# Optimization experiments

Measured on AMD Instinct MI355X. Metric: run time of the kernel, lower is better.

Reference implementation:

```python
import jax, jax.numpy as jnp
import numpy as np

B, N, Th, Td, Tw, Tp = 8, 3000, 24, 12, 24, 12
T2a, T2b, K = 64, 32, 3  # hidden temporal dims of the two STBlocks, Cheb order


def _laplacian(A):
    # PyG ChebConv with lambda_max=None -> lambda_max=2.0, sym normalization:
    # L_hat = 2L/lambda_max - I = -D^{-1/2} A D^{-1/2} with zero diagonal
    Aod = A * (1.0 - jnp.eye(A.shape[0], dtype=A.dtype))
    deg = Aod.sum(axis=1)
    dinv = jnp.where(deg > 0, deg ** -0.5, 0.0)
    return -(dinv[:, None] * Aod * dinv[None, :])


def _cheb(x, L, W, b):
    # Chebyshev graph conv, K=3. x: (B,N,Cin), L: (N,N), W: (K,Cin,Cout), b: (Cout,)
    Tx0 = x
    Tx1 = jnp.einsum('nm,bmi->bni', L, Tx0)
    Tx2 = 2.0 * jnp.einsum('nm,bmi->bni', L, Tx1) - Tx0
    out = (jnp.einsum('bni,io->bno', Tx0, W[0])
           + jnp.einsum('bni,io->bno', Tx1, W[1])
           + jnp.einsum('bni,io->bno', Tx2, W[2]))
    return out + b


def _tconv(x, w, b):
    # Conv1d(1, 1, 3, padding=1) over last axis. x: (B,N,T), w: (3,), b: scalar
    xp = jnp.pad(x, ((0, 0), (0, 0), (1, 1)))
    return w[0] * xp[..., :-2] + w[1] * xp[..., 1:-1] + w[2] * xp[..., 2:] + b


def _stblock(x, L, W, bg, cw, cb):
    x = jax.nn.relu(_cheb(x, L, W, bg))
    return jax.nn.relu(_tconv(x, cw, cb))


def _branch(X, L, W1, b1, c1w, c1b, W2, b2, c2w, c2b, WD, bD):
    x = X.reshape(X.shape[0], X.shape[1], X.shape[3])  # (B,N,T)
    x = _stblock(x, L, W1, b1, c1w, c1b)  # (B,N,64)
    x = _stblock(x, L, W2, b2, c2w, c2b)  # (B,N,32)
    return jax.nn.relu(x @ WD + bD)       # (B,N,Tp); forward only uses LinearD


def setup_inputs() -> dict:
    ks = jax.random.split(jax.random.key(0), 48)
    it = iter(range(48))

    def nrm(shape, s=1.0):
        return jax.random.normal(ks[next(it)], shape, jnp.float32) * s

    Xh = nrm((B, N, 1, Th))
    Xd = nrm((B, N, 1, Td))
    Xw = nrm((B, N, 1, Tw))
    u = jax.random.uniform(ks[next(it)], (N, N))
    w = jax.random.uniform(ks[next(it)], (N, N))
    A = jnp.where(u < 0.01, w, 0.0)
    A = 0.5 * (A + A.T)

    def gcn_p(ti, to):
        return nrm((K, ti, to), (2.0 / (ti + to)) ** 0.5), jnp.zeros((to,), jnp.float32)

    def conv_p():
        return nrm((K,), 0.4), nrm((), 0.1)

    Wh1, bh1 = gcn_p(Th, T2a); ch1w, ch1b = conv_p()
    Wh2, bh2 = gcn_p(T2a, T2b); ch2w, ch2b = conv_p()
    Wd1, bd1 = gcn_p(Td, T2a); cd1w, cd1b = conv_p()
    Wd2, bd2 = gcn_p(T2a, T2b); cd2w, cd2b = conv_p()
    Ww1, bw1 = gcn_p(Tw, T2a); cw1w, cw1b = conv_p()
    Ww2, bw2 = gcn_p(T2a, T2b); cw2w, cw2b = conv_p()
    WD = nrm((T2b, Tp), (2.0 / (T2b + Tp)) ** 0.5)
    bD = jnp.zeros((Tp,), jnp.float32)
    Fh = jax.random.uniform(ks[next(it)], (Tp,), jnp.float32)
    Fd = jax.random.uniform(ks[next(it)], (Tp,), jnp.float32)
    Fw = jax.random.uniform(ks[next(it)], (Tp,), jnp.float32)

    return dict(Xh=Xh, Xd=Xd, Xw=Xw, A=A,
                Wh1=Wh1, bh1=bh1, ch1w=ch1w, ch1b=ch1b, Wh2=Wh2, bh2=bh2, ch2w=ch2w, ch2b=ch2b,
                Wd1=Wd1, bd1=bd1, cd1w=cd1w, cd1b=cd1b, Wd2=Wd2, bd2=bd2, cd2w=cd2w, cd2b=cd2b,
                Ww1=Ww1, bw1=bw1, cw1w=cw1w, cw1b=cw1b, Ww2=Ww2, bw2=bw2, cw2w=cw2w, cw2b=cw2b,
                WD=WD, bD=bD, Fh=Fh, Fd=Fd, Fw=Fw)


def reference(Xh, Xd, Xw, A,
              Wh1, bh1, ch1w, ch1b, Wh2, bh2, ch2w, ch2b,
              Wd1, bd1, cd1w, cd1b, Wd2, bd2, cd2w, cd2b,
              Ww1, bw1, cw1w, cw1b, Ww2, bw2, cw2w, cw2b,
              WD, bD, Fh, Fd, Fw):
    L = _laplacian(A)
    Yh = _branch(Xh, L, Wh1, bh1, ch1w, ch1b, Wh2, bh2, ch2w, ch2b, WD, bD)
    Yd = _branch(Xd, L, Wd1, bd1, cd1w, cd1b, Wd2, bd2, cd2w, cd2b, WD, bD)
    Yw = _branch(Xw, L, Ww1, bw1, cw1w, cw1b, Ww2, bw2, cw2w, cw2b, WD, bD)
    Y = Fh * Yh + Fd * Yd + Fw * Yw  # Fusion: elementwise weighted sum over Tp
    return Y[:, :, None, :]  # (B,N,1,Tp)
```

## Files before the change

### kernel.cpp

```cpp
#include <hip/hip_runtime.h>

#define NN 3000
#define NB 8
#define TP 12
#define DMAX 128
#define F1T 480
#define F2T 768
#define Z1T 1536

struct BrW {
    const float *W1[3]; const float *b1[3]; const float *c1w[3]; const float *c1b[3];
    const float *W2[3]; const float *b2[3]; const float *c2w[3]; const float *c2b[3];
    const float *Fb[3];
};

__global__ void build_kernel(const float* __restrict__ A, int* __restrict__ colp,
                             float* __restrict__ valp, int* __restrict__ cnt,
                             float* __restrict__ dinv) {
    int n = blockIdx.x;
    int lane = threadIdx.x;
    const float* row = A + (size_t)n * NN;
    int base = 0;
    float s = 0.f;
    for (int start = 0; start < NN; start += 64) {
        int m = start + lane;
        float a = 0.f; bool nz = false;
        if (m < NN && m != n) {
            a = row[m];
            nz = (a != 0.f);
        }
        s += a;
        unsigned long long mask = __ballot(nz);
        int off = __popcll(mask & ((1ull << lane) - 1ull));
        if (nz) {
            int idx = base + off;
            if (idx < DMAX) { colp[n * DMAX + idx] = m; valp[n * DMAX + idx] = a; }
        }
        base += __popcll(mask);
    }
    for (int o = 32; o > 0; o >>= 1) s += __shfl_down(s, o);
    if (lane == 0) {
        cnt[n] = (base < DMAX) ? base : DMAX;
        dinv[n] = (s > 0.f) ? 1.0f / sqrtf(s) : 0.f;
    }
}

__global__ void scale_kernel(const int* __restrict__ colp, float* __restrict__ valp,
                             const int* __restrict__ cnt, const float* __restrict__ dinv) {
    int n = blockIdx.x;
    int j = threadIdx.x;
    if (j < cnt[n]) {
        int m = colp[n * DMAX + j];
        valp[n * DMAX + j] *= -dinv[n] * dinv[m];
    }
}

__global__ void pack_kernel(const float* __restrict__ Xh, const float* __restrict__ Xd,
                            const float* __restrict__ Xw, float* __restrict__ xcat) {
    int idx = blockIdx.x * blockDim.x + threadIdx.x;
    if (idx >= NN * F1T) return;
    int n = idx / F1T, r = idx % F1T;
    const float* src; int b, t, T;
    if (r < 192)      { src = Xh; T = 24; int rr = r;       b = rr / 24; t = rr % 24; }
    else if (r < 288) { src = Xd; T = 12; int rr = r - 192; b = rr / 12; t = rr % 12; }
    else              { src = Xw; T = 24; int rr = r - 288; b = rr / 24; t = rr % 24; }
    xcat[idx] = src[((size_t)b * NN + n) * T + t];
}

template <int F, int SLICE, int EPI>
__global__ void spmm_kernel(const int* __restrict__ colp, const float* __restrict__ valp,
                            const int* __restrict__ cnt, const float* __restrict__ x,
                            const float* __restrict__ aux, float* __restrict__ y) {
    int nwg = gridDim.x;
    int q = nwg >> 3;
    int bid = blockIdx.x;
    int w = (bid & 7) * q + (bid >> 3);
    int slice = w / NN;
    int n = w - slice * NN;
    int f = slice * SLICE + threadIdx.x;

    __shared__ int   scol[DMAX];
    __shared__ float sval[DMAX];
    int c = cnt[n];
    if (threadIdx.x < DMAX) {
        int j = threadIdx.x;
        bool ok = j < c;
        scol[j] = ok ? colp[n * DMAX + j] * F : 0;
        sval[j] = ok ? valp[n * DMAX + j] : 0.f;
    }
    __syncthreads();
    int c32 = (c + 31) & ~31;
    float a0 = 0.f, a1 = 0.f, a2 = 0.f, a3 = 0.f;
    float a4 = 0.f, a5 = 0.f, a6 = 0.f, a7 = 0.f;
    if (f < F) {
        for (int i = 0; i < c32; i += 32) {
            float g[32], w32[32];
            #pragma unroll
            for (int u = 0; u < 32; ++u) {
                int cc = scol[i + u];
                w32[u] = sval[i + u];
                g[u] = x[cc + f];
            }
            #pragma unroll
            for (int u = 0; u < 32; u += 8) {
                a0 += w32[u + 0] * g[u + 0]; a1 += w32[u + 1] * g[u + 1];
                a2 += w32[u + 2] * g[u + 2]; a3 += w32[u + 3] * g[u + 3];
                a4 += w32[u + 4] * g[u + 4]; a5 += w32[u + 5] * g[u + 5];
                a6 += w32[u + 6] * g[u + 6]; a7 += w32[u + 7] * g[u + 7];
            }
        }
    }
    if (f >= F) return;
    float acc = ((a0 + a1) + (a2 + a3)) + ((a4 + a5) + (a6 + a7));
    size_t o = (size_t)n * F + f;
    if (EPI == 1) acc = 2.f * acc - aux[o];
    else if (EPI == 2) acc = aux[o] + 2.f * acc;
    y[o] = acc;
}

#define SZ_LDA 68
template <int T, int OFF>
__device__ __forceinline__ void fused1_body(
        int tile, int br, const float* __restrict__ xcat, const float* __restrict__ t1cat,
        const float* __restrict__ t2cat, float* __restrict__ y1cat,
        float* __restrict__ y2cat, float* __restrict__ c0cat, const BrW& P, float* smem) {
    constexpr int K = 3 * T;
    constexpr int LDA = K + 1;
    int tid = threadIdx.x;
    float* sW1 = smem;
    float* sX  = smem + K * 64;
    const float* W1 = P.W1[br];
    for (int i = tid; i < K * 64; i += 256) sW1[i] = W1[i];
    int n0 = tile * 12;
    #pragma unroll
    for (int s = 0; s < 3; ++s) {
        const float* src = (s == 0) ? xcat : (s == 1) ? t1cat : t2cat;
        for (int i = tid; i < 96 * T; i += 256) {
            int n_l = i / (8 * T), rem = i % (8 * T);
            int b = rem / T, ii = rem % T;
            sX[(n_l * 8 + b) * LDA + s * T + ii] =
                src[(size_t)(n0 + n_l) * F1T + OFF + b * T + ii];
        }
    }
    __syncthreads();

    int rq = tid >> 3;
    int g  = tid & 7;
    float acc[3][8];
    #pragma unroll
    for (int r = 0; r < 3; ++r)
        #pragma unroll
        for (int j = 0; j < 8; ++j) acc[r][j] = 0.f;

    #pragma unroll 4
    for (int k = 0; k < K; ++k) {
        const float4* wr = reinterpret_cast<const float4*>(sW1 + k * 64 + g * 8);
        float4 wa = wr[0], wb = wr[1];
        #pragma unroll
        for (int r = 0; r < 3; ++r) {
            float zv = sX[(rq * 3 + r) * LDA + k];
            acc[r][0] += zv * wa.x; acc[r][1] += zv * wa.y;
            acc[r][2] += zv * wa.z; acc[r][3] += zv * wa.w;
            acc[r][4] += zv * wb.x; acc[r][5] += zv * wb.y;
            acc[r][6] += zv * wb.z; acc[r][7] += zv * wb.w;
        }
    }

    float bgv[8];
    #pragma unroll
    for (int j = 0; j < 8; ++j) bgv[j] = P.b1[br][g * 8 + j];
    float w0 = P.c1w[br][0], w1 = P.c1w[br][1], w2 = P.c1w[br][2], bb = P.c1b[br][0];

    float o[3][8];
    #pragma unroll
    for (int r = 0; r < 3; ++r) {
        float z[8];
        #pragma unroll
        for (int j = 0; j < 8; ++j) z[j] = fmaxf(acc[r][j] + bgv[j], 0.f);
        float zl = __shfl_up(z[7], 1);
        float zr = __shfl_down(z[0], 1);
        #pragma unroll
        for (int j = 0; j < 8; ++j) {
            float left  = (j > 0) ? z[j - 1] : ((g > 0) ? zl : 0.f);
            float right = (j < 7) ? z[j + 1] : ((g < 7) ? zr : 0.f);
            o[r][j] = fmaxf(w0 * left + w1 * z[j] + w2 * right + bb, 0.f);
        }
    }
    __syncthreads();

    float* sZ  = smem;
    float* sW2 = smem + 96 * SZ_LDA;
    #pragma unroll
    for (int r = 0; r < 3; ++r) {
        float* dst = sZ + (rq * 3 + r) * SZ_LDA + g * 8;
        reinterpret_cast<float4*>(dst)[0] = make_float4(o[r][0], o[r][1], o[r][2], o[r][3]);
        reinterpret_cast<float4*>(dst)[1] = make_float4(o[r][4], o[r][5], o[r][6], o[r][7]);
    }
    const float* W2 = P.W2[br];
    for (int i = tid; i < 6144; i += 256) {
        int k = i / 96, cc = i % 96;
        int j = cc / 3, m = cc % 3;
        sW2[i] = W2[m * 2048 + k * 32 + j];
    }
    __syncthreads();

    float acc2[3][12];
    #pragma unroll
    for (int r = 0; r < 3; ++r)
        #pragma unroll
        for (int j = 0; j < 12; ++j) acc2[r][j] = 0.f;

    #pragma unroll 4
    for (int k = 0; k < 64; ++k) {
        const float4* wr = reinterpret_cast<const float4*>(sW2 + k * 96 + g * 12);
        float4 wa = wr[0], wb = wr[1], wc = wr[2];
        #pragma unroll
        for (int r = 0; r < 3; ++r) {
            float zv = sZ[(rq * 3 + r) * SZ_LDA + k];
            acc2[r][0] += zv * wa.x;  acc2[r][1] += zv * wa.y;
            acc2[r][2] += zv * wa.z;  acc2[r][3] += zv * wa.w;
            acc2[r][4] += zv * wb.x;  acc2[r][5] += zv * wb.y;
            acc2[r][6] += zv * wb.z;  acc2[r][7] += zv * wb.w;
            acc2[r][8] += zv * wc.x;  acc2[r][9] += zv * wc.y;
            acc2[r][10] += zv * wc.z; acc2[r][11] += zv * wc.w;
        }
    }

    const float* b2 = P.b2[br];
    #pragma unroll
    for (int r = 0; r < 3; ++r) {
        int unit = tile * 96 + rq * 3 + r;
        int n = unit >> 3, b = unit & 7;
        size_t obase = (size_t)n * F2T + br * 256 + b * 32;
        #pragma unroll
        for (int jj = 0; jj < 4; ++jj) {
            int j = g * 4 + jj;
            float a0 = acc2[r][jj * 3 + 0], a1 = acc2[r][jj * 3 + 1], a2 = acc2[r][jj * 3 + 2];
            y1cat[obase + j] = a1;
            y2cat[obase + j] = a2;
            c0cat[obase + j] = a0 - a2 + b2[j];
        }
    }
}

__global__ void __launch_bounds__(256)
fused1_kernel(const float* __restrict__ xcat, const float* __restrict__ t1cat,
              const float* __restrict__ t2cat, float* __restrict__ y1cat,
              float* __restrict__ y2cat, float* __restrict__ c0cat, BrW P) {
    __shared__ float smem[12672];
    int b = blockIdx.x;
    if (b < 250)      fused1_body<24, 0>(b, 0, xcat, t1cat, t2cat, y1cat, y2cat, c0cat, P, smem);
    else if (b < 500) fused1_body<12, 192>(b - 250, 1, xcat, t1cat, t2cat, y1cat, y2cat, c0cat, P, smem);
    else              fused1_body<24, 288>(b - 500, 2, xcat, t1cat, t2cat, y1cat, y2cat, c0cat, P, smem);
}

__global__ void combine2_final_kernel(const float* __restrict__ c0cat,
                                      const float* __restrict__ vcat,
                                      const float* __restrict__ WD, const float* __restrict__ bD,
                                      float* __restrict__ out, BrW P) {
    int n = blockIdx.x;
    __shared__ float z2[3][NB][32];
    int unit = threadIdx.x >> 5;
    int co = threadIdx.x & 31;
    int br = unit >> 3, b = unit & 7;
    size_t o = (size_t)n * F2T + br * 256 + b * 32 + co;
    float a = fmaxf(c0cat[o] + vcat[o], 0.f);
    float left  = __shfl_up(a, 1);
    float right = __shfl_down(a, 1);
    if (co == 0) left = 0.f;
    if (co == 31) right = 0.f;
    float w0 = P.c2w[br][0], w1 = P.c2w[br][1], w2 = P.c2w[br][2], bb = P.c2b[br][0];
    z2[br][b][co] = fmaxf(w0 * left + w1 * a + w2 * right + bb, 0.f);
    __syncthreads();
    if (threadIdx.x < NB * TP) {
        int b2 = threadIdx.x / TP, tp = threadIdx.x % TP;
        float y = 0.f;
        for (int brr = 0; brr < 3; ++brr) {
            float s = bD[tp];
            const float* zz = z2[brr][b2];
            for (int c = 0; c < 32; ++c) s += zz[c] * WD[c * TP + tp];
            y += fmaxf(s, 0.f) * P.Fb[brr][tp];
        }
        out[((size_t)b2 * NN + n) * TP + tp] = y;
    }
}


static inline size_t align256(size_t x) { return (x + 255) & ~(size_t)255; }

extern "C" void kernel_launch(void* const* d_in, const int* in_sizes, int n_in,
                              void* d_out, int out_size, void* d_ws, size_t ws_size,
                              hipStream_t stream) {
    const float* Xh = (const float*)d_in[0];
    const float* Xd = (const float*)d_in[1];
    const float* Xw = (const float*)d_in[2];
    const float* A  = (const float*)d_in[3];
    const float* WD = (const float*)d_in[28];
    const float* bD = (const float*)d_in[29];

    BrW P;
    for (int br = 0; br < 3; ++br) {
        int base = 4 + br * 8;
        P.W1[br]  = (const float*)d_in[base + 0];
        P.b1[br]  = (const float*)d_in[base + 1];
        P.c1w[br] = (const float*)d_in[base + 2];
        P.c1b[br] = (const float*)d_in[base + 3];
        P.W2[br]  = (const float*)d_in[base + 4];
        P.b2[br]  = (const float*)d_in[base + 5];
        P.c2w[br] = (const float*)d_in[base + 6];
        P.c2b[br] = (const float*)d_in[base + 7];
        P.Fb[br]  = (const float*)d_in[30 + br];
    }

    char* p = (char*)d_ws;
    int*   colp  = (int*)p;   p += align256((size_t)NN * DMAX * 4);
    float* valp  = (float*)p; p += align256((size_t)NN * DMAX * 4);
    int*   cnt   = (int*)p;   p += align256(NN * 4);
    float* dinv  = (float*)p; p += align256(NN * 4);
    float* xcat  = (float*)p; p += align256((size_t)NN * F1T * 4);
    float* t1cat = (float*)p; p += align256((size_t)NN * F1T * 4);
    float* t2cat = (float*)p; p += align256((size_t)NN * F1T * 4);
    float* y1cat = (float*)p; p += align256((size_t)NN * F2T * 4);
    float* y2cat = (float*)p; p += align256((size_t)NN * F2T * 4);
    float* c0cat = (float*)p; p += align256((size_t)NN * F2T * 4);
    float* scat  = (float*)p; p += align256((size_t)NN * F2T * 4);
    float* vcat  = (float*)p; p += align256((size_t)NN * F2T * 4);

    build_kernel<<<NN, 64, 0, stream>>>(A, colp, valp, cnt, dinv);
    scale_kernel<<<NN, DMAX, 0, stream>>>(colp, valp, cnt, dinv);
    pack_kernel<<<(NN * F1T + 255) / 256, 256, 0, stream>>>(Xh, Xd, Xw, xcat);

    spmm_kernel<F1T, 256, 0><<<6000, 256, 0, stream>>>(colp, valp, cnt, xcat, nullptr, t1cat);
    spmm_kernel<F1T, 256, 1><<<6000, 256, 0, stream>>>(colp, valp, cnt, t1cat, xcat, t2cat);

    fused1_kernel<<<750, 256, 0, stream>>>(xcat, t1cat, t2cat, y1cat, y2cat, c0cat, P);

    spmm_kernel<F2T, 128, 2><<<18000, 128, 0, stream>>>(colp, valp, cnt, y2cat, y1cat, scat);
    spmm_kernel<F2T, 128, 0><<<18000, 128, 0, stream>>>(colp, valp, cnt, scat, nullptr, vcat);

    combine2_final_kernel<<<NN, 768, 0, stream>>>(c0cat, vcat, WD, bD, (float*)d_out, P);
}
```

Before: 175.4 us.

## Fuse final SpMM into combine, merge scale/pack, retile fused1, vectorize adjacency scan

The last SpMM over the second-block features is folded into the final combine kernel, so one launch and the vcat write/read round trip go away. The scale and pack kernels become a single launch. fused1 moves to 192 threads with 4 rows per thread and an odd shared-memory stride, plus launch bounds asking for two blocks per CU. build_kernel now reads the adjacency with float4 loads. The trade-offs are that the final kernel uses one 768-thread block per node with no slicing, and fused1 holds more registers per thread.

```diff
diff --git a/kernel.cpp b/kernel.cpp
--- a/kernel.cpp
+++ b/kernel.cpp
@@ -6,7 +6,6 @@
 #define DMAX 128
 #define F1T 480
 #define F2T 768
-#define Z1T 1536
 
 struct BrW {
     const float *W1[3]; const float *b1[3]; const float *c1w[3]; const float *c1b[3];
@@ -19,24 +18,29 @@
                              float* __restrict__ dinv) {
     int n = blockIdx.x;
     int lane = threadIdx.x;
-    const float* row = A + (size_t)n * NN;
+    const float4* row4 = reinterpret_cast<const float4*>(A + (size_t)n * NN);
     int base = 0;
     float s = 0.f;
-    for (int start = 0; start < NN; start += 64) {
-        int m = start + lane;
-        float a = 0.f; bool nz = false;
-        if (m < NN && m != n) {
-            a = row[m];
-            nz = (a != 0.f);
-        }
-        s += a;
-        unsigned long long mask = __ballot(nz);
-        int off = __popcll(mask & ((1ull << lane) - 1ull));
-        if (nz) {
-            int idx = base + off;
-            if (idx < DMAX) { colp[n * DMAX + idx] = m; valp[n * DMAX + idx] = a; }
-        }
-        base += __popcll(mask);
+    for (int start = 0; start < 750; start += 64) {
+        int m4 = start + lane;
+        float4 v = make_float4(0.f, 0.f, 0.f, 0.f);
+        if (m4 < 750) v = row4[m4];
+        float vals[4] = {v.x, v.y, v.z, v.w};
+        int mbase = m4 * 4;
+        #pragma unroll
+        for (int u = 0; u < 4; ++u) {
+            int m = mbase + u;
+            float a = (m4 < 750 && m != n) ? vals[u] : 0.f;
+            bool nz = (a != 0.f);
+            s += a;
+            unsigned long long mask = __ballot(nz);
+            int off = __popcll(mask & ((1ull << lane) - 1ull));
+            if (nz) {
+                int idx = base + off;
+                if (idx < DMAX) { colp[n * DMAX + idx] = m; valp[n * DMAX + idx] = a; }
+            }
+            base += __popcll(mask);
+        }
     }
     for (int o = 32; o > 0; o >>= 1) s += __shfl_down(s, o);
     if (lane == 0) {
@@ -45,26 +49,28 @@
     }
 }
 
-__global__ void scale_kernel(const int* __restrict__ colp, float* __restrict__ valp,
-                             const int* __restrict__ cnt, const float* __restrict__ dinv) {
-    int n = blockIdx.x;
-    int j = threadIdx.x;
-    if (j < cnt[n]) {
-        int m = colp[n * DMAX + j];
-        valp[n * DMAX + j] *= -dinv[n] * dinv[m];
-    }
-}
-
-__global__ void pack_kernel(const float* __restrict__ Xh, const float* __restrict__ Xd,
-                            const float* __restrict__ Xw, float* __restrict__ xcat) {
-    int idx = blockIdx.x * blockDim.x + threadIdx.x;
-    if (idx >= NN * F1T) return;
-    int n = idx / F1T, r = idx % F1T;
-    const float* src; int b, t, T;
-    if (r < 192)      { src = Xh; T = 24; int rr = r;       b = rr / 24; t = rr % 24; }
-    else if (r < 288) { src = Xd; T = 12; int rr = r - 192; b = rr / 12; t = rr % 12; }
-    else              { src = Xw; T = 24; int rr = r - 288; b = rr / 24; t = rr % 24; }
-    xcat[idx] = src[((size_t)b * NN + n) * T + t];
+__global__ void scale_pack_kernel(const int* __restrict__ colp, float* __restrict__ valp,
+                                  const int* __restrict__ cnt, const float* __restrict__ dinv,
+                                  const float* __restrict__ Xh, const float* __restrict__ Xd,
+                                  const float* __restrict__ Xw, float* __restrict__ xcat) {
+    int bid = blockIdx.x;
+    if (bid < NN) {
+        int n = bid;
+        int j = threadIdx.x;
+        if (j < DMAX && j < cnt[n]) {
+            int m = colp[n * DMAX + j];
+            valp[n * DMAX + j] *= -dinv[n] * dinv[m];
+        }
+    } else {
+        int idx = (bid - NN) * 256 + threadIdx.x;
+        if (idx >= NN * F1T) return;
+        int n = idx / F1T, r = idx % F1T;
+        const float* src; int b, t, T;
+        if (r < 192)      { src = Xh; T = 24; int rr = r;       b = rr / 24; t = rr % 24; }
+        else if (r < 288) { src = Xd; T = 12; int rr = r - 192; b = rr / 12; t = rr % 12; }
+        else              { src = Xw; T = 24; int rr = r - 288; b = rr / 24; t = rr % 24; }
+        xcat[idx] = src[((size_t)b * NN + n) * T + t];
+    }
 }
 
 template <int F, int SLICE, int EPI>
@@ -118,7 +124,7 @@
     y[o] = acc;
 }
 
-#define SZ_LDA 68
+#define SZ_LDA 67
 template <int T, int OFF>
 __device__ __forceinline__ void fused1_body(
         int tile, int br, const float* __restrict__ xcat, const float* __restrict__ t1cat,
@@ -130,12 +136,12 @@
     float* sW1 = smem;
     float* sX  = smem + K * 64;
     const float* W1 = P.W1[br];
-    for (int i = tid; i < K * 64; i += 256) sW1[i] = W1[i];
+    for (int i = tid; i < K * 64; i += 192) sW1[i] = W1[i];
     int n0 = tile * 12;
     #pragma unroll
     for (int s = 0; s < 3; ++s) {
         const float* src = (s == 0) ? xcat : (s == 1) ? t1cat : t2cat;
-        for (int i = tid; i < 96 * T; i += 256) {
+        for (int i = tid; i < 96 * T; i += 192) {
             int n_l = i / (8 * T), rem = i % (8 * T);
             int b = rem / T, ii = rem % T;
             sX[(n_l * 8 + b) * LDA + s * T + ii] =
@@ -146,9 +152,9 @@
 
     int rq = tid >> 3;
     int g  = tid & 7;
-    float acc[3][8];
-    #pragma unroll
-    for (int r = 0; r < 3; ++r)
+    float acc[4][8];
+    #pragma unroll
+    for (int r = 0; r < 4; ++r)
         #pragma unroll
         for (int j = 0; j < 8; ++j) acc[r][j] = 0.f;
 
@@ -157,8 +163,8 @@
         const float4* wr = reinterpret_cast<const float4*>(sW1 + k * 64 + g * 8);
         float4 wa = wr[0], wb = wr[1];
         #pragma unroll
-        for (int r = 0; r < 3; ++r) {
-            float zv = sX[(rq * 3 + r) * LDA + k];
+        for (int r = 0; r < 4; ++r) {
+            float zv = sX[(rq * 4 + r) * LDA + k];
             acc[r][0] += zv * wa.x; acc[r][1] += zv * wa.y;
             acc[r][2] += zv * wa.z; acc[r][3] += zv * wa.w;
             acc[r][4] += zv * wb.x; acc[r][5] += zv * wb.y;
@@ -171,9 +177,9 @@
     for (int j = 0; j < 8; ++j) bgv[j] = P.b1[br][g * 8 + j];
     float w0 = P.c1w[br][0], w1 = P.c1w[br][1], w2 = P.c1w[br][2], bb = P.c1b[br][0];
 
-    float o[3][8];
-    #pragma unroll
-    for (int r = 0; r < 3; ++r) {
+    float o[4][8];
+    #pragma unroll
+    for (int r = 0; r < 4; ++r) {
         float z[8];
         #pragma unroll
         for (int j = 0; j < 8; ++j) z[j] = fmaxf(acc[r][j] + bgv[j], 0.f);
@@ -191,22 +197,22 @@
     float* sZ  = smem;
     float* sW2 = smem + 96 * SZ_LDA;
     #pragma unroll
-    for (int r = 0; r < 3; ++r) {
-        float* dst = sZ + (rq * 3 + r) * SZ_LDA + g * 8;
-        reinterpret_cast<float4*>(dst)[0] = make_float4(o[r][0], o[r][1], o[r][2], o[r][3]);
-        reinterpret_cast<float4*>(dst)[1] = make_float4(o[r][4], o[r][5], o[r][6], o[r][7]);
+    for (int r = 0; r < 4; ++r) {
+        float* dst = sZ + (rq * 4 + r) * SZ_LDA + g * 8;
+        #pragma unroll
+        for (int j = 0; j < 8; ++j) dst[j] = o[r][j];
     }
     const float* W2 = P.W2[br];
-    for (int i = tid; i < 6144; i += 256) {
+    for (int i = tid; i < 6144; i += 192) {
         int k = i / 96, cc = i % 96;
         int j = cc / 3, m = cc % 3;
         sW2[i] = W2[m * 2048 + k * 32 + j];
     }
     __syncthreads();
 
-    float acc2[3][12];
-    #pragma unroll
-    for (int r = 0; r < 3; ++r)
+    float acc2[4][12];
+    #pragma unroll
+    for (int r = 0; r < 4; ++r)
         #pragma unroll
         for (int j = 0; j < 12; ++j) acc2[r][j] = 0.f;
 
@@ -215,8 +221,8 @@
         const float4* wr = reinterpret_cast<const float4*>(sW2 + k * 96 + g * 12);
         float4 wa = wr[0], wb = wr[1], wc = wr[2];
         #pragma unroll
-        for (int r = 0; r < 3; ++r) {
-            float zv = sZ[(rq * 3 + r) * SZ_LDA + k];
+        for (int r = 0; r < 4; ++r) {
+            float zv = sZ[(rq * 4 + r) * SZ_LDA + k];
             acc2[r][0] += zv * wa.x;  acc2[r][1] += zv * wa.y;
             acc2[r][2] += zv * wa.z;  acc2[r][3] += zv * wa.w;
             acc2[r][4] += zv * wb.x;  acc2[r][5] += zv * wb.y;
@@ -228,8 +234,8 @@
 
     const float* b2 = P.b2[br];
     #pragma unroll
-    for (int r = 0; r < 3; ++r) {
-        int unit = tile * 96 + rq * 3 + r;
+    for (int r = 0; r < 4; ++r) {
+        int unit = tile * 96 + rq * 4 + r;
         int n = unit >> 3, b = unit & 7;
         size_t obase = (size_t)n * F2T + br * 256 + b * 32;
         #pragma unroll
@@ -243,28 +249,62 @@
     }
 }
 
-__global__ void __launch_bounds__(256)
+__global__ void __launch_bounds__(192, 2)
 fused1_kernel(const float* __restrict__ xcat, const float* __restrict__ t1cat,
               const float* __restrict__ t2cat, float* __restrict__ y1cat,
               float* __restrict__ y2cat, float* __restrict__ c0cat, BrW P) {
-    __shared__ float smem[12672];
+    __shared__ float smem[12576];
     int b = blockIdx.x;
     if (b < 250)      fused1_body<24, 0>(b, 0, xcat, t1cat, t2cat, y1cat, y2cat, c0cat, P, smem);
     else if (b < 500) fused1_body<12, 192>(b - 250, 1, xcat, t1cat, t2cat, y1cat, y2cat, c0cat, P, smem);
     else              fused1_body<24, 288>(b - 500, 2, xcat, t1cat, t2cat, y1cat, y2cat, c0cat, P, smem);
 }
 
-__global__ void combine2_final_kernel(const float* __restrict__ c0cat,
-                                      const float* __restrict__ vcat,
-                                      const float* __restrict__ WD, const float* __restrict__ bD,
-                                      float* __restrict__ out, BrW P) {
-    int n = blockIdx.x;
+__global__ void __launch_bounds__(768)
+spmm_final_kernel(const int* __restrict__ colp, const float* __restrict__ valp,
+                  const int* __restrict__ cnt, const float* __restrict__ x,
+                  const float* __restrict__ c0cat, const float* __restrict__ WD,
+                  const float* __restrict__ bD, float* __restrict__ out, BrW P) {
+    int bid = blockIdx.x;
+    int n = (bid & 7) * (NN / 8) + (bid >> 3);
+    int f = threadIdx.x;
+
+    __shared__ int   scol[DMAX];
+    __shared__ float sval[DMAX];
     __shared__ float z2[3][NB][32];
-    int unit = threadIdx.x >> 5;
-    int co = threadIdx.x & 31;
+    int c = cnt[n];
+    if (threadIdx.x < DMAX) {
+        int j = threadIdx.x;
+        bool ok = j < c;
+        scol[j] = ok ? colp[n * DMAX + j] * F2T : 0;
+        sval[j] = ok ? valp[n * DMAX + j] : 0.f;
+    }
+    __syncthreads();
+    int c32 = (c + 31) & ~31;
+    float a0 = 0.f, a1 = 0.f, a2 = 0.f, a3 = 0.f;
+    float a4 = 0.f, a5 = 0.f, a6 = 0.f, a7 = 0.f;
+    for (int i = 0; i < c32; i += 32) {
+        float g[32], w32[32];
+        #pragma unroll
+        for (int u = 0; u < 32; ++u) {
+            int cc = scol[i + u];
+            w32[u] = sval[i + u];
+            g[u] = x[cc + f];
+        }
+        #pragma unroll
+        for (int u = 0; u < 32; u += 8) {
+            a0 += w32[u + 0] * g[u + 0]; a1 += w32[u + 1] * g[u + 1];
+            a2 += w32[u + 2] * g[u + 2]; a3 += w32[u + 3] * g[u + 3];
+            a4 += w32[u + 4] * g[u + 4]; a5 += w32[u + 5] * g[u + 5];
+            a6 += w32[u + 6] * g[u + 6]; a7 += w32[u + 7] * g[u + 7];
+        }
+    }
+    float v = ((a0 + a1) + (a2 + a3)) + ((a4 + a5) + (a6 + a7));
+
+    int co = f & 31;
+    int unit = f >> 5;
     int br = unit >> 3, b = unit & 7;
-    size_t o = (size_t)n * F2T + br * 256 + b * 32 + co;
-    float a = fmaxf(c0cat[o] + vcat[o], 0.f);
+    float a = fmaxf(c0cat[(size_t)n * F2T + f] + v, 0.f);
     float left  = __shfl_up(a, 1);
     float right = __shfl_down(a, 1);
     if (co == 0) left = 0.f;
@@ -272,13 +312,14 @@
     float w0 = P.c2w[br][0], w1 = P.c2w[br][1], w2 = P.c2w[br][2], bb = P.c2b[br][0];
     z2[br][b][co] = fmaxf(w0 * left + w1 * a + w2 * right + bb, 0.f);
     __syncthreads();
+
     if (threadIdx.x < NB * TP) {
         int b2 = threadIdx.x / TP, tp = threadIdx.x % TP;
         float y = 0.f;
         for (int brr = 0; brr < 3; ++brr) {
             float s = bD[tp];
             const float* zz = z2[brr][b2];
-            for (int c = 0; c < 32; ++c) s += zz[c] * WD[c * TP + tp];
+            for (int cc = 0; cc < 32; ++cc) s += zz[cc] * WD[cc * TP + tp];
             y += fmaxf(s, 0.f) * P.Fb[brr][tp];
         }
         out[((size_t)b2 * NN + n) * TP + tp] = y;
@@ -324,19 +365,17 @@
     float* y2cat = (float*)p; p += align256((size_t)NN * F2T * 4);
     float* c0cat = (float*)p; p += align256((size_t)NN * F2T * 4);
     float* scat  = (float*)p; p += align256((size_t)NN * F2T * 4);
-    float* vcat  = (float*)p; p += align256((size_t)NN * F2T * 4);
 
     build_kernel<<<NN, 64, 0, stream>>>(A, colp, valp, cnt, dinv);
-    scale_kernel<<<NN, DMAX, 0, stream>>>(colp, valp, cnt, dinv);
-    pack_kernel<<<(NN * F1T + 255) / 256, 256, 0, stream>>>(Xh, Xd, Xw, xcat);
+    scale_pack_kernel<<<NN + (NN * F1T + 255) / 256, 256, 0, stream>>>(
+        colp, valp, cnt, dinv, Xh, Xd, Xw, xcat);
 
     spmm_kernel<F1T, 256, 0><<<6000, 256, 0, stream>>>(colp, valp, cnt, xcat, nullptr, t1cat);
     spmm_kernel<F1T, 256, 1><<<6000, 256, 0, stream>>>(colp, valp, cnt, t1cat, xcat, t2cat);
 
-    fused1_kernel<<<750, 256, 0, stream>>>(xcat, t1cat, t2cat, y1cat, y2cat, c0cat, P);
+    fused1_kernel<<<750, 192, 0, stream>>>(xcat, t1cat, t2cat, y1cat, y2cat, c0cat, P);
 
     spmm_kernel<F2T, 128, 2><<<18000, 128, 0, stream>>>(colp, valp, cnt, y2cat, y1cat, scat);
-    spmm_kernel<F2T, 128, 0><<<18000, 128, 0, stream>>>(colp, valp, cnt, scat, nullptr, vcat);
-
-    combine2_final_kernel<<<NN, 768, 0, stream>>>(c0cat, vcat, WD, bD, (float*)d_out, P);
-}
+    spmm_final_kernel<<<NN, 768, 0, stream>>>(colp, valp, cnt, scat, c0cat, WD, bD,
+                                              (float*)d_out, P);
+}
```

Measured after the change: 195.1 us. 11.2% more time.
